# Kernel optimization log

Hardware: AMD Instinct MI355X
Metric: run time of the kernel (lower is better)

Reference implementation:

```python
import jax, jax.numpy as jnp
import numpy as np

SIGMA = 0.05  # gaussian bandwidth from the source


def _sqdist(a, b):
    # a: [B,N,D], b: [B,M,D] -> [B,N,M] squared euclidean distance
    a2 = jnp.sum(a * a, axis=-1)[:, :, None]
    b2 = jnp.sum(b * b, axis=-1)[:, None, :]
    return a2 + b2 - 2.0 * jnp.einsum('bnd,bmd->bnm', a, b)


def setup_inputs() -> dict:
    key = jax.random.key(0)
    k1, k2, k3, k4 = jax.random.split(key, 4)
    B, N, D = 2, 4096, 32
    points = jax.random.normal(k1, (B, N, 3), dtype=jnp.float32)
    pointfea1 = jax.random.normal(k2, (B, N, D), dtype=jnp.float32)
    pointfea2 = jax.random.normal(k3, (B, N, D), dtype=jnp.float32)
    weights = jax.random.uniform(k4, (B, N), dtype=jnp.float32) / N  # point-cloud mass weights
    return {"points": points, "pointfea1": pointfea1, "pointfea2": pointfea2, "weights": weights}


def reference(points, pointfea1, pointfea2, weights):
    # naive_corres: per-point spatial log-gaussian softmax vs feature log-softmax,
    # weighted squared difference, reduced over both pair axes -> [B]
    x = points / SIGMA
    point_loggauss = jax.nn.log_softmax(-_sqdist(x, x), axis=2)          # [B,N,N]
    fea_logsoftmax = jax.nn.log_softmax(-_sqdist(pointfea1, pointfea2), axis=2)  # [B,N,N]
    diff2 = (jnp.exp(point_loggauss) - jnp.exp(fea_logsoftmax)) ** 2
    l2_loss = jnp.sum(diff2 * weights[:, :, None], axis=2)  # sum over j
    return jnp.sum(l2_loss, axis=1)                          # sum over i -> [B]
```

## Files before the change

kernel.cpp:

```cpp
#include <hip/hip_runtime.h>

#define D    32
#define BLK  256
#define NCH  16
#define SJ   128

#define LOG2E 1.44269504088896340736f

typedef short  short8  __attribute__((ext_vector_type(8)));
typedef float  floatx4 __attribute__((ext_vector_type(4)));
typedef float  v2f     __attribute__((ext_vector_type(2)));

__device__ __forceinline__ short f2bf(float v) {
    union { float f; unsigned u; } x; x.f = v;
    unsigned r = x.u + 0x7fffu + ((x.u >> 16) & 1u);
    return (short)(r >> 16);
}
__device__ __forceinline__ float bf2f(short h) {
    union { float f; unsigned u; } x;
    x.u = ((unsigned)(unsigned short)h) << 16;
    return x.f;
}
__device__ __forceinline__ float fast_exp2(float x) {
#if __has_builtin(__builtin_amdgcn_exp2f)
    return __builtin_amdgcn_exp2f(x);
#else
    return exp2f(x);
#endif
}

__global__ __launch_bounds__(BLK) void precompute_kernel(
    const float* __restrict__ points,
    const float* __restrict__ fea1,
    const float* __restrict__ fea2,
    float4* __restrict__ xp,
    float* __restrict__ f1n,
    float* __restrict__ f2n,
    short* __restrict__ f2hi,
    short* __restrict__ f2lo,
    float* __restrict__ acc,
    float* __restrict__ out,
    int BN, int Bsz)
{
    int r = blockIdx.x * BLK + threadIdx.x;
    if (r < Bsz) out[r] = 0.0f;
    if (r >= BN) return;
#pragma unroll
    for (int s = 0; s < 5; ++s) acc[s * BN + r] = 0.0f;

    const float s20 = 20.0f;
    float x = points[3*r+0] * s20;
    float y = points[3*r+1] * s20;
    float z = points[3*r+2] * s20;
    float4 v; v.x = x; v.y = y; v.z = z;
    v.w = (x*x + y*y + z*z) * LOG2E;
    xp[r] = v;

    const float4* p1 = (const float4*)(fea1 + (size_t)r * D);
    float n1 = 0.f;
#pragma unroll
    for (int k = 0; k < D/4; ++k) {
        float4 a = p1[k];
        n1 = fmaf(a.x,a.x, fmaf(a.y,a.y, fmaf(a.z,a.z, fmaf(a.w,a.w, n1))));
    }
    f1n[r] = n1 * LOG2E;

    const int t = r >> 4;
    const int m = r & 15;
    const float* p2 = fea2 + (size_t)r * D;
    float n2 = 0.f;
#pragma unroll
    for (int q = 0; q < 4; ++q) {
        float4 v0 = *(const float4*)(p2 + q*8);
        float4 v1 = *(const float4*)(p2 + q*8 + 4);
        float e[8] = {v0.x,v0.y,v0.z,v0.w,v1.x,v1.y,v1.z,v1.w};
        short8 h, l;
#pragma unroll
        for (int k = 0; k < 8; ++k) {
            n2 = fmaf(e[k], e[k], n2);
            short hh = f2bf(e[k]);
            h[k] = hh;
            l[k] = f2bf(e[k] - bf2f(hh));
        }
        size_t off = ((size_t)t * 64 + m + 16*q) * 8;
        *(short8*)&f2hi[off] = h;
        *(short8*)&f2lo[off] = l;
    }
    f2n[r] = n2 * LOG2E;
}

__global__ __launch_bounds__(BLK) void pair_kernel(
    const float* __restrict__ fea1,
    const short* __restrict__ f2hi,
    const short* __restrict__ f2lo,
    const float4* __restrict__ xp,
    const float* __restrict__ f1n,
    const float* __restrict__ f2n,
    float* __restrict__ acc,
    int N, int BN)
{
    __shared__ __align__(16) short sHi[SJ * D];
    __shared__ __align__(16) short sLo[SJ * D];
    __shared__ float4 sXJ[SJ];
    __shared__ float  sFN[SJ];

    const int tid  = threadIdx.x;
    const int lane = tid & 63;
    const int wv   = tid >> 6;
    const int m    = lane & 15;
    const int q    = lane >> 4;

    const int ibpb  = N / 64;
    const int b     = blockIdx.x / ibpb;
    const int ibase = blockIdx.x * 64 + wv * 16;
    const int JCH   = N / NCH;
    const int jc0   = blockIdx.y * JCH;

    const float* f1p = fea1 + (size_t)(ibase + m) * D + q * 8;
    float4 bv0 = *(const float4*)(f1p);
    float4 bv1 = *(const float4*)(f1p + 4);
    float bf[8] = {bv0.x,bv0.y,bv0.z,bv0.w,bv1.x,bv1.y,bv1.z,bv1.w};
    short8 Bhi, Blo;
#pragma unroll
    for (int k = 0; k < 8; ++k) {
        short h = f2bf(bf[k]);
        Bhi[k] = h;
        Blo[k] = f2bf(bf[k] - bf2f(h));
    }

    const float L2 = 2.0f * LOG2E;
    float4 xi = xp[ibase + m];
    float xix = xi.x * L2, xiy = xi.y * L2, xiz = xi.z * L2;
    float mxiw = -xi.w;
    float nfi  = -f1n[ibase + m];

    v2f sAB = {0.f, 0.f};
    v2f s2  = {0.f, 0.f};
    float sab = 0.f;

    const short*  gHi  = f2hi + ((size_t)(b * N + jc0) >> 4) * 512;
    const short*  gLo  = f2lo + ((size_t)(b * N + jc0) >> 4) * 512;
    const float4* xpb  = xp  + (size_t)b * N + jc0;
    const float*  f2nb = f2n + (size_t)b * N + jc0;

    for (int s = 0; s < JCH; s += SJ) {
        const uint4* srcH = (const uint4*)(gHi + (size_t)(s >> 4) * 512);
        const uint4* srcL = (const uint4*)(gLo + (size_t)(s >> 4) * 512);
        uint4* dstH = (uint4*)sHi;
        uint4* dstL = (uint4*)sLo;
        dstH[tid]       = srcH[tid];
        dstH[tid + 256] = srcH[tid + 256];
        dstL[tid]       = srcL[tid];
        dstL[tid + 256] = srcL[tid + 256];
        if (tid < SJ) {
            sXJ[tid] = xpb[s + tid];
            sFN[tid] = f2nb[s + tid];
        }
        __syncthreads();

#pragma unroll 2
        for (int jt8 = 0; jt8 < SJ/16; ++jt8) {
            const short8 Ahi = *(const short8*)&sHi[(jt8 * 64 + lane) * 8];
            const short8 Alo = *(const short8*)&sLo[(jt8 * 64 + lane) * 8];
            floatx4 c = {0.f, 0.f, 0.f, 0.f};
            c = __builtin_amdgcn_mfma_f32_16x16x32_bf16(Ahi, Bhi, c, 0, 0, 0);
            c = __builtin_amdgcn_mfma_f32_16x16x32_bf16(Ahi, Blo, c, 0, 0, 0);
            c = __builtin_amdgcn_mfma_f32_16x16x32_bf16(Alo, Bhi, c, 0, 0, 0);
#pragma unroll
            for (int r = 0; r < 4; ++r) {
                int jl = jt8 * 16 + q * 4 + r;
                float4 xj = sXJ[jl];
                float bL = fmaf(c[r], L2, nfi - sFN[jl]);
                float aL = fmaf(xiz, xj.z,
                             fmaf(xiy, xj.y,
                              fmaf(xix, xj.x, mxiw))) - xj.w;
                float ea = fast_exp2(aL);
                float eb = fast_exp2(bL);
                v2f e = {ea, eb};
                sAB += e;
                s2   = __builtin_elementwise_fma(e, e, s2);
                sab  = fmaf(ea, eb, sab);
            }
        }
        __syncthreads();
    }

    float vA = sAB.x, vB = sAB.y, v2a = s2.x, v2b = s2.y, vab = sab;
    vA  += __shfl_xor(vA, 16);  vA  += __shfl_xor(vA, 32);
    vB  += __shfl_xor(vB, 16);  vB  += __shfl_xor(vB, 32);
    v2a += __shfl_xor(v2a, 16); v2a += __shfl_xor(v2a, 32);
    v2b += __shfl_xor(v2b, 16); v2b += __shfl_xor(v2b, 32);
    vab += __shfl_xor(vab, 16); vab += __shfl_xor(vab, 32);

    if (lane < 16) {
        int row = ibase + lane;
        atomicAdd(&acc[0*BN + row], vA);
        atomicAdd(&acc[1*BN + row], v2a);
        atomicAdd(&acc[2*BN + row], vB);
        atomicAdd(&acc[3*BN + row], v2b);
        atomicAdd(&acc[4*BN + row], vab);
    }
}

__global__ __launch_bounds__(BLK) void finalize_kernel(
    const float* __restrict__ acc,
    const float* __restrict__ weights,
    float* __restrict__ out,
    int N, int BN)
{
    int row = blockIdx.x * BLK + threadIdx.x;
    int b   = (blockIdx.x * BLK) / N;

    float A   = acc[0*BN + row];
    float S2a = acc[1*BN + row];
    float Bt  = acc[2*BN + row];
    float S2b = acc[3*BN + row];
    float Sab = acc[4*BN + row];
    float invA = 1.0f / A;
    float invB = 1.0f / Bt;
    float val  = S2a*invA*invA - 2.0f*Sab*invA*invB + S2b*invB*invB;
    float sum  = weights[row] * val;

    __shared__ float red[BLK/64];
    for (int off = 32; off > 0; off >>= 1)
        sum += __shfl_down(sum, off);
    if ((threadIdx.x & 63) == 0) red[threadIdx.x >> 6] = sum;
    __syncthreads();
    if (threadIdx.x == 0) {
        float s = 0.f;
#pragma unroll
        for (int w = 0; w < BLK/64; ++w) s += red[w];
        atomicAdd(&out[b], s);
    }
}

extern "C" void kernel_launch(void* const* d_in, const int* in_sizes, int n_in,
                              void* d_out, int out_size, void* d_ws, size_t ws_size,
                              hipStream_t stream) {
    const float* points  = (const float*)d_in[0];
    const float* fea1    = (const float*)d_in[1];
    const float* fea2    = (const float*)d_in[2];
    const float* weights = (const float*)d_in[3];
    float* out = (float*)d_out;

    int B  = out_size;
    int BN = in_sizes[3];
    int N  = BN / B;

    float*  acc  = (float*)d_ws;
    float4* xp   = (float4*)((char*)d_ws + (size_t)5  * BN * 4);
    float*  f2n  = (float*)((char*)d_ws + (size_t)9  * BN * 4);
    float*  f1n  = (float*)((char*)d_ws + (size_t)10 * BN * 4);
    short*  f2hi = (short*)((char*)d_ws + (size_t)11 * BN * 4);
    short*  f2lo = f2hi + (size_t)BN * D;

    precompute_kernel<<<dim3((BN + BLK - 1) / BLK), dim3(BLK), 0, stream>>>(
        points, fea1, fea2, xp, f1n, f2n, f2hi, f2lo, acc, out, BN, B);

    dim3 grid(BN / 64, NCH);
    pair_kernel<<<grid, dim3(BLK), 0, stream>>>(
        fea1, f2hi, f2lo, xp, f1n, f2n, acc, N, BN);

    finalize_kernel<<<dim3(BN / BLK), dim3(BLK), 0, stream>>>(acc, weights, out, N, BN);
}
```

Baseline: 84.78 us.

## Drop LDS staging; read interleaved j-tiles directly from global with register prefetch

The pair kernel stops staging the fea2 bf16 hi/lo tiles and the per-j point/norm data through shared memory behind __syncthreads. It now reads them straight from global memory (L2/L1 cached) in a new interleaved layout: hi and lo tiles adjacent, and per-tile x/y/z/-w/-norm packed as float4 rows. The next tile's MFMA operands are prefetched into registers. The epilogue math is also rewritten as packed 2-wide float ops. This removes the barrier and LDS traffic, at the cost of relying on cache hits for data every wave rereads and of more live registers.

```diff
diff --git a/kernel.cpp b/kernel.cpp
--- a/kernel.cpp
+++ b/kernel.cpp
@@ -3,7 +3,6 @@
 #define D    32
 #define BLK  256
 #define NCH  16
-#define SJ   128
 
 #define LOG2E 1.44269504088896340736f
 
@@ -35,9 +34,8 @@
     const float* __restrict__ fea2,
     float4* __restrict__ xp,
     float* __restrict__ f1n,
-    float* __restrict__ f2n,
-    short* __restrict__ f2hi,
-    short* __restrict__ f2lo,
+    float* __restrict__ jpk,
+    short* __restrict__ f2ab,
     float* __restrict__ acc,
     float* __restrict__ out,
     int BN, int Bsz)
@@ -82,28 +80,28 @@
             h[k] = hh;
             l[k] = f2bf(e[k] - bf2f(hh));
         }
-        size_t off = ((size_t)t * 64 + m + 16*q) * 8;
-        *(short8*)&f2hi[off] = h;
-        *(short8*)&f2lo[off] = l;
-    }
-    f2n[r] = n2 * LOG2E;
+        size_t off = (size_t)t * 1024 + (size_t)(m + 16*q) * 8;
+        *(short8*)&f2ab[off]       = h;
+        *(short8*)&f2ab[off + 512] = l;
+    }
+
+    float* jb = jpk + (size_t)t * 80 + m;
+    jb[0]  = v.x;
+    jb[16] = v.y;
+    jb[32] = v.z;
+    jb[48] = -v.w;
+    jb[64] = -n2 * LOG2E;
 }
 
 __global__ __launch_bounds__(BLK) void pair_kernel(
     const float* __restrict__ fea1,
-    const short* __restrict__ f2hi,
-    const short* __restrict__ f2lo,
+    const short* __restrict__ f2ab,
+    const float* __restrict__ jpk,
     const float4* __restrict__ xp,
     const float* __restrict__ f1n,
-    const float* __restrict__ f2n,
     float* __restrict__ acc,
     int N, int BN)
 {
-    __shared__ __align__(16) short sHi[SJ * D];
-    __shared__ __align__(16) short sLo[SJ * D];
-    __shared__ float4 sXJ[SJ];
-    __shared__ float  sFN[SJ];
-
     const int tid  = threadIdx.x;
     const int lane = tid & 63;
     const int wv   = tid >> 6;
@@ -115,6 +113,7 @@
     const int ibase = blockIdx.x * 64 + wv * 16;
     const int JCH   = N / NCH;
     const int jc0   = blockIdx.y * JCH;
+    const int JT    = JCH >> 4;
 
     const float* f1p = fea1 + (size_t)(ibase + m) * D + q * 8;
     float4 bv0 = *(const float4*)(f1p);
@@ -130,62 +129,87 @@
 
     const float L2 = 2.0f * LOG2E;
     float4 xi = xp[ibase + m];
-    float xix = xi.x * L2, xiy = xi.y * L2, xiz = xi.z * L2;
-    float mxiw = -xi.w;
-    float nfi  = -f1n[ibase + m];
-
-    v2f sAB = {0.f, 0.f};
-    v2f s2  = {0.f, 0.f};
-    float sab = 0.f;
-
-    const short*  gHi  = f2hi + ((size_t)(b * N + jc0) >> 4) * 512;
-    const short*  gLo  = f2lo + ((size_t)(b * N + jc0) >> 4) * 512;
-    const float4* xpb  = xp  + (size_t)b * N + jc0;
-    const float*  f2nb = f2n + (size_t)b * N + jc0;
-
-    for (int s = 0; s < JCH; s += SJ) {
-        const uint4* srcH = (const uint4*)(gHi + (size_t)(s >> 4) * 512);
-        const uint4* srcL = (const uint4*)(gLo + (size_t)(s >> 4) * 512);
-        uint4* dstH = (uint4*)sHi;
-        uint4* dstL = (uint4*)sLo;
-        dstH[tid]       = srcH[tid];
-        dstH[tid + 256] = srcH[tid + 256];
-        dstL[tid]       = srcL[tid];
-        dstL[tid + 256] = srcL[tid + 256];
-        if (tid < SJ) {
-            sXJ[tid] = xpb[s + tid];
-            sFN[tid] = f2nb[s + tid];
-        }
-        __syncthreads();
-
-#pragma unroll 2
-        for (int jt8 = 0; jt8 < SJ/16; ++jt8) {
-            const short8 Ahi = *(const short8*)&sHi[(jt8 * 64 + lane) * 8];
-            const short8 Alo = *(const short8*)&sLo[(jt8 * 64 + lane) * 8];
-            floatx4 c = {0.f, 0.f, 0.f, 0.f};
-            c = __builtin_amdgcn_mfma_f32_16x16x32_bf16(Ahi, Bhi, c, 0, 0, 0);
-            c = __builtin_amdgcn_mfma_f32_16x16x32_bf16(Ahi, Blo, c, 0, 0, 0);
-            c = __builtin_amdgcn_mfma_f32_16x16x32_bf16(Alo, Bhi, c, 0, 0, 0);
-#pragma unroll
-            for (int r = 0; r < 4; ++r) {
-                int jl = jt8 * 16 + q * 4 + r;
-                float4 xj = sXJ[jl];
-                float bL = fmaf(c[r], L2, nfi - sFN[jl]);
-                float aL = fmaf(xiz, xj.z,
-                             fmaf(xiy, xj.y,
-                              fmaf(xix, xj.x, mxiw))) - xj.w;
-                float ea = fast_exp2(aL);
-                float eb = fast_exp2(bL);
-                v2f e = {ea, eb};
-                sAB += e;
-                s2   = __builtin_elementwise_fma(e, e, s2);
-                sab  = fmaf(ea, eb, sab);
-            }
-        }
-        __syncthreads();
-    }
-
-    float vA = sAB.x, vB = sAB.y, v2a = s2.x, v2b = s2.y, vab = sab;
+    float nfi = -f1n[ibase + m];
+    v2f vxx = {xi.x * L2, xi.x * L2};
+    v2f vxy = {xi.y * L2, xi.y * L2};
+    v2f vxz = {xi.z * L2, xi.z * L2};
+    v2f vmw = {-xi.w, -xi.w};
+    v2f vnf = {nfi, nfi};
+    v2f vL2 = {L2, L2};
+
+    v2f sA  = {0.f, 0.f};
+    v2f sB  = {0.f, 0.f};
+    v2f s2a = {0.f, 0.f};
+    v2f s2b = {0.f, 0.f};
+    v2f sab = {0.f, 0.f};
+
+    const size_t tg0 = (size_t)(b * N + jc0) >> 4;
+    const short* pA  = f2ab + tg0 * 1024 + (size_t)lane * 8;
+    const float* pJ  = jpk  + tg0 * 80   + (size_t)q * 4;
+
+    short8 Ah = *(const short8*)(pA);
+    short8 Al = *(const short8*)(pA + 512);
+
+#define DO_GROUP(c2, x2, y2, z2, w2, f2)                                 \
+    do {                                                                 \
+        v2f t0 = __builtin_elementwise_fma(x2, vxx, vmw);                \
+        t0 = __builtin_elementwise_fma(y2, vxy, t0);                     \
+        t0 = __builtin_elementwise_fma(z2, vxz, t0);                     \
+        v2f aL = t0 + (w2);                                              \
+        v2f bL = __builtin_elementwise_fma(c2, vL2, vnf + (f2));         \
+        v2f ea; ea.x = fast_exp2(aL.x); ea.y = fast_exp2(aL.y);          \
+        v2f eb; eb.x = fast_exp2(bL.x); eb.y = fast_exp2(bL.y);          \
+        sA += ea;                                                        \
+        sB += eb;                                                        \
+        s2a = __builtin_elementwise_fma(ea, ea, s2a);                    \
+        s2b = __builtin_elementwise_fma(eb, eb, s2b);                    \
+        sab = __builtin_elementwise_fma(ea, eb, sab);                    \
+    } while (0)
+
+    for (int t = 0; t < JT; ++t) {
+        const short* pAn = pA + (t + 1 < JT ? 1024 : 0);
+        short8 Ah1 = *(const short8*)(pAn);
+        short8 Al1 = *(const short8*)(pAn + 512);
+
+        const float* pj = pJ + (size_t)t * 80;
+        float4 X = *(const float4*)(pj);
+        float4 Y = *(const float4*)(pj + 16);
+        float4 Z = *(const float4*)(pj + 32);
+        float4 W = *(const float4*)(pj + 48);
+        float4 F = *(const float4*)(pj + 64);
+
+        floatx4 c = {0.f, 0.f, 0.f, 0.f};
+        c = __builtin_amdgcn_mfma_f32_16x16x32_bf16(Ah, Bhi, c, 0, 0, 0);
+        c = __builtin_amdgcn_mfma_f32_16x16x32_bf16(Ah, Blo, c, 0, 0, 0);
+        c = __builtin_amdgcn_mfma_f32_16x16x32_bf16(Al, Bhi, c, 0, 0, 0);
+
+        v2f c01; c01.x = c[0]; c01.y = c[1];
+        v2f c23; c23.x = c[2]; c23.y = c[3];
+        v2f x01; x01.x = X.x; x01.y = X.y;
+        v2f x23; x23.x = X.z; x23.y = X.w;
+        v2f y01; y01.x = Y.x; y01.y = Y.y;
+        v2f y23; y23.x = Y.z; y23.y = Y.w;
+        v2f z01; z01.x = Z.x; z01.y = Z.y;
+        v2f z23; z23.x = Z.z; z23.y = Z.w;
+        v2f w01; w01.x = W.x; w01.y = W.y;
+        v2f w23; w23.x = W.z; w23.y = W.w;
+        v2f f01; f01.x = F.x; f01.y = F.y;
+        v2f f23; f23.x = F.z; f23.y = F.w;
+
+        DO_GROUP(c01, x01, y01, z01, w01, f01);
+        DO_GROUP(c23, x23, y23, z23, w23, f23);
+
+        pA = pAn;
+        Ah = Ah1; Al = Al1;
+    }
+#undef DO_GROUP
+
+    float vA  = sA.x  + sA.y;
+    float vB  = sB.x  + sB.y;
+    float v2a = s2a.x + s2a.y;
+    float v2b = s2b.x + s2b.y;
+    float vab = sab.x + sab.y;
+
     vA  += __shfl_xor(vA, 16);  vA  += __shfl_xor(vA, 32);
     vB  += __shfl_xor(vB, 16);  vB  += __shfl_xor(vB, 32);
     v2a += __shfl_xor(v2a, 16); v2a += __shfl_xor(v2a, 32);
@@ -249,17 +273,16 @@
 
     float*  acc  = (float*)d_ws;
     float4* xp   = (float4*)((char*)d_ws + (size_t)5  * BN * 4);
-    float*  f2n  = (float*)((char*)d_ws + (size_t)9  * BN * 4);
-    float*  f1n  = (float*)((char*)d_ws + (size_t)10 * BN * 4);
-    short*  f2hi = (short*)((char*)d_ws + (size_t)11 * BN * 4);
-    short*  f2lo = f2hi + (size_t)BN * D;
+    float*  f1n  = (float*)((char*)d_ws + (size_t)9  * BN * 4);
+    float*  jpk  = (float*)((char*)d_ws + (size_t)10 * BN * 4);
+    short*  f2ab = (short*)((char*)d_ws + (size_t)15 * BN * 4);
 
     precompute_kernel<<<dim3((BN + BLK - 1) / BLK), dim3(BLK), 0, stream>>>(
-        points, fea1, fea2, xp, f1n, f2n, f2hi, f2lo, acc, out, BN, B);
+        points, fea1, fea2, xp, f1n, jpk, f2ab, acc, out, BN, B);
 
     dim3 grid(BN / 64, NCH);
     pair_kernel<<<grid, dim3(BLK), 0, stream>>>(
-        fea1, f2hi, f2lo, xp, f1n, f2n, acc, N, BN);
+        fea1, f2ab, jpk, xp, f1n, acc, N, BN);
 
     finalize_kernel<<<dim3(BN / BLK), dim3(BLK), 0, stream>>>(acc, weights, out, N, BN);
 }
```

After: 97.27 us. 1.15x slower.

## Transpose MFMA operands so each lane holds four i-rows and one j column

Applied to the files above, without the earlier changes.

Swaps the A/B operands of the bf16 MFMA so the output accumulator lanes map to four consecutive i rows per lane and one j column, instead of four j columns for one i. Each lane now loads a single j's coordinates and norm from LDS per tile rather than four, and the per-row i parameters are kept in packed two-wide vectors so the exp arguments and accumulations can use packed FMA. The end-of-kernel reduction changes to a cross-lane shuffle over the 16 j lanes, and lanes pick their row's value before the atomics. The cost is more accumulator registers per lane and a longer final shuffle reduction.

```diff
diff --git a/kernel.cpp b/kernel.cpp
--- a/kernel.cpp
+++ b/kernel.cpp
@@ -119,24 +119,36 @@
     const float* f1p = fea1 + (size_t)(ibase + m) * D + q * 8;
     float4 bv0 = *(const float4*)(f1p);
     float4 bv1 = *(const float4*)(f1p + 4);
-    float bf[8] = {bv0.x,bv0.y,bv0.z,bv0.w,bv1.x,bv1.y,bv1.z,bv1.w};
-    short8 Bhi, Blo;
+    float bfv[8] = {bv0.x,bv0.y,bv0.z,bv0.w,bv1.x,bv1.y,bv1.z,bv1.w};
+    short8 F1hi, F1lo;
 #pragma unroll
     for (int k = 0; k < 8; ++k) {
-        short h = f2bf(bf[k]);
-        Bhi[k] = h;
-        Blo[k] = f2bf(bf[k] - bf2f(h));
+        short h = f2bf(bfv[k]);
+        F1hi[k] = h;
+        F1lo[k] = f2bf(bfv[k] - bf2f(h));
     }
 
     const float L2 = 2.0f * LOG2E;
-    float4 xi = xp[ibase + m];
-    float xix = xi.x * L2, xiy = xi.y * L2, xiz = xi.z * L2;
-    float mxiw = -xi.w;
-    float nfi  = -f1n[ibase + m];
-
-    v2f sAB = {0.f, 0.f};
-    v2f s2  = {0.f, 0.f};
-    float sab = 0.f;
+    v2f vxx[2], vxy[2], vxz[2], vmw[2], vnf[2];
+#pragma unroll
+    for (int g = 0; g < 2; ++g) {
+        int i0 = ibase + q*4 + g*2;
+        float4 a0 = xp[i0];
+        float4 a1 = xp[i0 + 1];
+        v2f t;
+        t.x = a0.x * L2; t.y = a1.x * L2; vxx[g] = t;
+        t.x = a0.y * L2; t.y = a1.y * L2; vxy[g] = t;
+        t.x = a0.z * L2; t.y = a1.z * L2; vxz[g] = t;
+        t.x = -a0.w;     t.y = -a1.w;     vmw[g] = t;
+        t.x = -f1n[i0];  t.y = -f1n[i0+1]; vnf[g] = t;
+    }
+    v2f vL2 = {L2, L2};
+
+    v2f sA2[2]  = {{0.f,0.f},{0.f,0.f}};
+    v2f sB2[2]  = {{0.f,0.f},{0.f,0.f}};
+    v2f s2a2[2] = {{0.f,0.f},{0.f,0.f}};
+    v2f s2b2[2] = {{0.f,0.f},{0.f,0.f}};
+    v2f sab2[2] = {{0.f,0.f},{0.f,0.f}};
 
     const short*  gHi  = f2hi + ((size_t)(b * N + jc0) >> 4) * 512;
     const short*  gLo  = f2lo + ((size_t)(b * N + jc0) >> 4) * 512;
@@ -163,42 +175,61 @@
             const short8 Ahi = *(const short8*)&sHi[(jt8 * 64 + lane) * 8];
             const short8 Alo = *(const short8*)&sLo[(jt8 * 64 + lane) * 8];
             floatx4 c = {0.f, 0.f, 0.f, 0.f};
-            c = __builtin_amdgcn_mfma_f32_16x16x32_bf16(Ahi, Bhi, c, 0, 0, 0);
-            c = __builtin_amdgcn_mfma_f32_16x16x32_bf16(Ahi, Blo, c, 0, 0, 0);
-            c = __builtin_amdgcn_mfma_f32_16x16x32_bf16(Alo, Bhi, c, 0, 0, 0);
-#pragma unroll
-            for (int r = 0; r < 4; ++r) {
-                int jl = jt8 * 16 + q * 4 + r;
-                float4 xj = sXJ[jl];
-                float bL = fmaf(c[r], L2, nfi - sFN[jl]);
-                float aL = fmaf(xiz, xj.z,
-                             fmaf(xiy, xj.y,
-                              fmaf(xix, xj.x, mxiw))) - xj.w;
-                float ea = fast_exp2(aL);
-                float eb = fast_exp2(bL);
-                v2f e = {ea, eb};
-                sAB += e;
-                s2   = __builtin_elementwise_fma(e, e, s2);
-                sab  = fmaf(ea, eb, sab);
+            c = __builtin_amdgcn_mfma_f32_16x16x32_bf16(F1hi, Ahi, c, 0, 0, 0);
+            c = __builtin_amdgcn_mfma_f32_16x16x32_bf16(F1hi, Alo, c, 0, 0, 0);
+            c = __builtin_amdgcn_mfma_f32_16x16x32_bf16(F1lo, Ahi, c, 0, 0, 0);
+
+            const int jl = jt8 * 16 + m;
+            float4 xj = sXJ[jl];
+            float fnj = sFN[jl];
+            v2f xx = {xj.x, xj.x};
+            v2f yy = {xj.y, xj.y};
+            v2f zz = {xj.z, xj.z};
+            v2f ww = {xj.w, xj.w};
+            v2f ff = {fnj, fnj};
+
+#pragma unroll
+            for (int g = 0; g < 2; ++g) {
+                v2f c2; c2.x = c[g*2]; c2.y = c[g*2 + 1];
+                v2f t0 = __builtin_elementwise_fma(xx, vxx[g], vmw[g]);
+                t0 = __builtin_elementwise_fma(yy, vxy[g], t0);
+                t0 = __builtin_elementwise_fma(zz, vxz[g], t0);
+                v2f aL = t0 - ww;
+                v2f bL = __builtin_elementwise_fma(c2, vL2, vnf[g] - ff);
+                v2f ea; ea.x = fast_exp2(aL.x); ea.y = fast_exp2(aL.y);
+                v2f eb; eb.x = fast_exp2(bL.x); eb.y = fast_exp2(bL.y);
+                sA2[g]  += ea;
+                sB2[g]  += eb;
+                s2a2[g] = __builtin_elementwise_fma(ea, ea, s2a2[g]);
+                s2b2[g] = __builtin_elementwise_fma(eb, eb, s2b2[g]);
+                sab2[g] = __builtin_elementwise_fma(ea, eb, sab2[g]);
             }
         }
         __syncthreads();
     }
 
-    float vA = sAB.x, vB = sAB.y, v2a = s2.x, v2b = s2.y, vab = sab;
-    vA  += __shfl_xor(vA, 16);  vA  += __shfl_xor(vA, 32);
-    vB  += __shfl_xor(vB, 16);  vB  += __shfl_xor(vB, 32);
-    v2a += __shfl_xor(v2a, 16); v2a += __shfl_xor(v2a, 32);
-    v2b += __shfl_xor(v2b, 16); v2b += __shfl_xor(v2b, 32);
-    vab += __shfl_xor(vab, 16); vab += __shfl_xor(vab, 32);
-
-    if (lane < 16) {
-        int row = ibase + lane;
-        atomicAdd(&acc[0*BN + row], vA);
-        atomicAdd(&acc[1*BN + row], v2a);
-        atomicAdd(&acc[2*BN + row], vB);
-        atomicAdd(&acc[3*BN + row], v2b);
-        atomicAdd(&acc[4*BN + row], vab);
+#define RED2(v) do {                                                       \
+        v.x += __shfl_xor(v.x, 1); v.x += __shfl_xor(v.x, 2);              \
+        v.x += __shfl_xor(v.x, 4); v.x += __shfl_xor(v.x, 8);              \
+        v.y += __shfl_xor(v.y, 1); v.y += __shfl_xor(v.y, 2);              \
+        v.y += __shfl_xor(v.y, 4); v.y += __shfl_xor(v.y, 8);              \
+    } while (0)
+#pragma unroll
+    for (int g = 0; g < 2; ++g) {
+        RED2(sA2[g]); RED2(s2a2[g]); RED2(sB2[g]); RED2(s2b2[g]); RED2(sab2[g]);
+    }
+#undef RED2
+
+    if (m < 4) {
+        int row = ibase + q*4 + m;
+#define PICK(arr) ((m & 1) ? ((m & 2) ? arr[1].y : arr[0].y)               \
+                           : ((m & 2) ? arr[1].x : arr[0].x))
+        atomicAdd(&acc[0*BN + row], PICK(sA2));
+        atomicAdd(&acc[1*BN + row], PICK(s2a2));
+        atomicAdd(&acc[2*BN + row], PICK(sB2));
+        atomicAdd(&acc[3*BN + row], PICK(s2b2));
+        atomicAdd(&acc[4*BN + row], PICK(sab2));
+#undef PICK
     }
 }
 
```

New measurement: 88.86 us. 1.05x slower.
